# Kernel optimization log

Hardware: AMD Instinct MI355X
Metric: run time of the kernel (lower is better)

Reference implementation:

```python
import jax, jax.numpy as jnp
import numpy as np

DIM_V, DIM_T, DIM_OUT, NUM_HEADS = 1024, 1024, 1024, 16
HEAD_DIM = DIM_OUT // NUM_HEADS
BETA = 1.0  # module multiplies scores by self.beta (=1); self.scale is unused


def setup_inputs() -> dict:
    key = jax.random.key(0)
    ks = jax.random.split(key, 12)
    B, N1, N2 = 8, 256, 4096
    E = jax.random.normal(ks[0], (B, N1, DIM_T), dtype=jnp.float32)
    I = jax.random.normal(ks[1], (B, N2, DIM_V), dtype=jnp.float32)
    s = 0.02
    # Conv1d(kernel_size=1) == linear; weights stored [out, in], bias [out]
    q_w = jax.random.normal(ks[2], (DIM_OUT, DIM_T), dtype=jnp.float32) * s
    q_b = jnp.zeros((DIM_OUT,), dtype=jnp.float32)
    k_w = jax.random.normal(ks[3], (DIM_OUT, DIM_V), dtype=jnp.float32) * s
    k_b = jnp.zeros((DIM_OUT,), dtype=jnp.float32)
    v_w = jax.random.normal(ks[4], (DIM_OUT, DIM_V), dtype=jnp.float32) * s
    v_b = jnp.zeros((DIM_OUT,), dtype=jnp.float32)
    p_w = jax.random.normal(ks[5], (DIM_OUT, DIM_OUT), dtype=jnp.float32) * s
    p_b = jnp.zeros((DIM_OUT,), dtype=jnp.float32)
    return {"E": E, "I": I, "q_w": q_w, "q_b": q_b, "k_w": k_w, "k_b": k_b,
            "v_w": v_w, "v_b": v_b, "p_w": p_w, "p_b": p_b}


def reference(E, I, q_w, q_b, k_w, k_b, v_w, v_b, p_w, p_b):
    B, N1, _ = E.shape
    _, N2, _ = I.shape
    # 1x1 conv projections == dense layers over channel dim
    Q = (jnp.einsum('bnc,oc->bno', E, q_w) + q_b).reshape(B, N1, NUM_HEADS, HEAD_DIM)
    K = (jnp.einsum('bmc,oc->bmo', I, k_w) + k_b).reshape(B, N2, NUM_HEADS, HEAD_DIM)
    V = (jnp.einsum('bmc,oc->bmo', I, v_w) + v_b).reshape(B, N2, NUM_HEADS, HEAD_DIM)
    # cross-attention scores [B, H, N1, N2]
    attn = jnp.einsum('bnhd,bmhd->bhnm', Q, K) * BETA
    attn = jax.nn.softmax(attn, axis=-1)
    U = jnp.einsum('bhnm,bmhd->bnhd', attn, V).reshape(B, N1, DIM_OUT)
    U = jnp.einsum('bnc,oc->bno', U, p_w) + p_b
    U = U / jnp.linalg.norm(U, axis=-1, keepdims=True)
    return jnp.concatenate([E, U], axis=2)  # [B, N1, dim_t + dim_out]
```

## Files before the change

### kernel.cpp

```cpp
#include <hip/hip_runtime.h>
#include <hip/hip_bf16.h>
#include <stdint.h>


typedef __bf16 bf16_t;
typedef __attribute__((ext_vector_type(8))) __bf16 bf16x8;
typedef __attribute__((ext_vector_type(4))) __bf16 bf16x4;
typedef __attribute__((ext_vector_type(4))) float f32x4;

#define DEVINL __device__ __forceinline__

DEVINL f32x4 mfma16(bf16x8 a, bf16x8 b, f32x4 c) {
  return __builtin_amdgcn_mfma_f32_16x16x32_bf16(a, b, c, 0, 0, 0);
}

DEVINL float fexp2(float x) { return __builtin_exp2f(x); }

DEVINL bf16x8 load8(const bf16_t* p) { return *(const bf16x8*)p; }
DEVINL bf16x8 load8(const float* p) {
  const float4 u = *(const float4*)p;
  const float4 v = *(const float4*)(p + 4);
  bf16x8 r;
  r[0] = (bf16_t)u.x; r[1] = (bf16_t)u.y; r[2] = (bf16_t)u.z; r[3] = (bf16_t)u.w;
  r[4] = (bf16_t)v.x; r[5] = (bf16_t)v.y; r[6] = (bf16_t)v.z; r[7] = (bf16_t)v.w;
  return r;
}

DEVINL uint32_t pack_bf16(float a, float b) {
  union { bf16_t h[2]; uint32_t u; } x;
  x.h[0] = (bf16_t)a; x.h[1] = (bf16_t)b;
  return x.u;
}

DEVINL void async16(const void* g, void* l) {
  typedef const __attribute__((address_space(1))) unsigned int* gp1;
  typedef __attribute__((address_space(3))) unsigned int* lp3;
  __builtin_amdgcn_global_load_lds((gp1)(uintptr_t)g,
                                   (lp3)(uint32_t)(uintptr_t)l, 16, 0, 0);
}

__global__ __launch_bounds__(256) void cvt_f32_bf16(
    const float* __restrict__ src, bf16_t* __restrict__ dst, int n8) {
  const int i = blockIdx.x * 256 + threadIdx.x;
  if (i < n8) *(bf16x8*)(dst + (size_t)i * 8) = load8(src + (size_t)i * 8);
}

template <int MODE>
__global__ __launch_bounds__(256) void gemm_bt_async(
    const bf16_t* __restrict__ A, const bf16_t* __restrict__ B,
    const float* __restrict__ bias, bf16_t* __restrict__ C,
    int M, int N, int K) {
  __shared__ bf16_t As[2][128 * 32];
  __shared__ bf16_t Bs[2][128 * 32];
  const int tid = threadIdx.x;
  const int w = tid >> 6, lane = tid & 63, quad = lane >> 4, l16 = lane & 15;
  const int bid = blockIdx.x;
  const int swz = (bid & 7) * (int)(gridDim.x >> 3) + (bid >> 3);
  const int big = swz >> 3, small = swz & 7;
  const int bm = 128 * (MODE == 1 ? small : big);
  const int bn = 128 * (MODE == 1 ? big : small);
  const int wm = (w & 1) * 64, wn = (w >> 1) * 64;
  const int srow = tid >> 2;
  const int sw8 = ((tid & 3) ^ (srow & 3)) * 8;

  const bf16_t* Ag0 = A + (size_t)(bm + srow) * K + sw8;
  const bf16_t* Ag1 = Ag0 + (size_t)64 * K;
  const bf16_t* Bg0 = B + (size_t)(bn + srow) * K + sw8;
  const bf16_t* Bg1 = Bg0 + (size_t)64 * K;

  f32x4 acc[4][4] = {};

  for (int k0 = 0; k0 < K; k0 += 64) {
    async16(Ag0 + k0, As[0] + tid * 8);
    async16(Ag1 + k0, As[0] + 64 * 32 + tid * 8);
    async16(Bg0 + k0, Bs[0] + tid * 8);
    async16(Bg1 + k0, Bs[0] + 64 * 32 + tid * 8);
    async16(Ag0 + k0 + 32, As[1] + tid * 8);
    async16(Ag1 + k0 + 32, As[1] + 64 * 32 + tid * 8);
    async16(Bg0 + k0 + 32, Bs[1] + tid * 8);
    async16(Bg1 + k0 + 32, Bs[1] + 64 * 32 + tid * 8);
    __syncthreads();
#pragma unroll
    for (int h = 0; h < 2; h++) {
      bf16x8 af[4], bfr[4];
#pragma unroll
      for (int mt = 0; mt < 4; mt++) {
        const int r = wm + mt * 16 + l16;
        af[mt] = *(const bf16x8*)(As[h] + r * 32 + ((quad ^ (r & 3)) * 8));
      }
#pragma unroll
      for (int nt = 0; nt < 4; nt++) {
        const int r = wn + nt * 16 + l16;
        bfr[nt] = *(const bf16x8*)(Bs[h] + r * 32 + ((quad ^ (r & 3)) * 8));
      }
#pragma unroll
      for (int mt = 0; mt < 4; mt++)
#pragma unroll
        for (int nt = 0; nt < 4; nt++)
          acc[mt][nt] = mfma16(af[mt], bfr[nt], acc[mt][nt]);
    }
    __syncthreads();
  }

#pragma unroll
  for (int mt = 0; mt < 4; mt++) {
#pragma unroll
    for (int nt = 0; nt < 4; nt++) {
      const int gm0 = bm + wm + mt * 16 + quad * 4;
      const int gn = bn + wn + nt * 16 + l16;
#pragma unroll
      for (int r = 0; r < 4; r++) {
        const int gm = gm0 + r;
        C[(size_t)gm * N + gn] =
            (bf16_t)(acc[mt][nt][r] + bias[MODE == 1 ? gm : gn]);
      }
    }
  }
}

template <int MODE, typename TA, typename TB>
__global__ __launch_bounds__(256) void gemm_bt_reg(
    const TA* __restrict__ A, const TB* __restrict__ B,
    const float* __restrict__ bias, void* __restrict__ Cv,
    int M, int N, int K) {
  __shared__ bf16_t As[128 * 32];
  __shared__ bf16_t Bs[128 * 32];
  const int tid = threadIdx.x;
  const int w = tid >> 6, lane = tid & 63, quad = lane >> 4, l16 = lane & 15;
  const int bm = blockIdx.x * 128, bn = blockIdx.y * 128;
  const int wm = (w & 1) * 64, wn = (w >> 1) * 64;
  const int srow = tid >> 2;
  const int swz = ((tid & 3) ^ (srow & 3)) * 8;

  const TA* Ag0 = A + (size_t)(bm + srow) * K + swz;
  const TA* Ag1 = Ag0 + (size_t)64 * K;
  const TB* Bg0 = B + (size_t)(bn + srow) * K + swz;
  const TB* Bg1 = Bg0 + (size_t)64 * K;
  bf16_t* Al0 = As + tid * 8;
  bf16_t* Al1 = As + 64 * 32 + tid * 8;
  bf16_t* Bl0 = Bs + tid * 8;
  bf16_t* Bl1 = Bs + 64 * 32 + tid * 8;

  f32x4 acc[4][4] = {};

  for (int k0 = 0; k0 < K; k0 += 32) {
    const bf16x8 a0 = load8(Ag0 + k0);
    const bf16x8 a1 = load8(Ag1 + k0);
    const bf16x8 b0 = load8(Bg0 + k0);
    const bf16x8 b1 = load8(Bg1 + k0);
    *(bf16x8*)Al0 = a0;
    *(bf16x8*)Al1 = a1;
    *(bf16x8*)Bl0 = b0;
    *(bf16x8*)Bl1 = b1;
    __syncthreads();
    bf16x8 af[4], bfr[4];
#pragma unroll
    for (int mt = 0; mt < 4; mt++) {
      const int r = wm + mt * 16 + l16;
      af[mt] = *(const bf16x8*)(As + r * 32 + ((quad ^ (r & 3)) * 8));
    }
#pragma unroll
    for (int nt = 0; nt < 4; nt++) {
      const int r = wn + nt * 16 + l16;
      bfr[nt] = *(const bf16x8*)(Bs + r * 32 + ((quad ^ (r & 3)) * 8));
    }
#pragma unroll
    for (int mt = 0; mt < 4; mt++)
#pragma unroll
      for (int nt = 0; nt < 4; nt++)
        acc[mt][nt] = mfma16(af[mt], bfr[nt], acc[mt][nt]);
    __syncthreads();
  }

#pragma unroll
  for (int mt = 0; mt < 4; mt++) {
#pragma unroll
    for (int nt = 0; nt < 4; nt++) {
      const int gm0 = bm + wm + mt * 16 + quad * 4;
      const int gn = bn + wn + nt * 16 + l16;
#pragma unroll
      for (int r = 0; r < 4; r++) {
        const int gm = gm0 + r;
        float v = acc[mt][nt][r] + bias[MODE == 1 ? gm : gn];
        if (MODE == 3) v *= 1.4426950408889634f;
        if (MODE == 2)
          ((float*)Cv)[(size_t)gm * N + gn] = v;
        else
          ((bf16_t*)Cv)[(size_t)gm * N + gn] = (bf16_t)v;
      }
    }
  }
}

DEVINL void attn_step2(bf16x8 ke0, bf16x8 ke1, bf16x8 ko0, bf16x8 ko1,
                       const bf16x8 (&vf)[4],
                       const bf16x8 (&qf0)[2], const bf16x8 (&qf1)[2],
                       f32x4 (&o)[4][2], float (&lacc)[2]) {
  const f32x4 cm44 = {-44.f, -44.f, -44.f, -44.f};
#pragma unroll
  for (int qg = 0; qg < 2; qg++) {
    f32x4 z0 = cm44;
    z0 = mfma16(ke0, qf0[qg], z0);
    const f32x4 ste = mfma16(ke1, qf1[qg], z0);
    f32x4 z1 = cm44;
    z1 = mfma16(ko0, qf0[qg], z1);
    const f32x4 sto = mfma16(ko1, qf1[qg], z1);
    const float pe0 = fexp2(ste[0]), pe1 = fexp2(ste[1]);
    const float pe2 = fexp2(ste[2]), pe3 = fexp2(ste[3]);
    const float po0 = fexp2(sto[0]), po1 = fexp2(sto[1]);
    const float po2 = fexp2(sto[2]), po3 = fexp2(sto[3]);
    lacc[qg] += ((pe0 + pe1) + (pe2 + pe3)) + ((po0 + po1) + (po2 + po3));
    union { uint32_t u[4]; bf16x8 v; } pb;
    pb.u[0] = pack_bf16(pe0, pe1);
    pb.u[1] = pack_bf16(pe2, pe3);
    pb.u[2] = pack_bf16(po0, po1);
    pb.u[3] = pack_bf16(po2, po3);
    o[0][qg] = mfma16(vf[0], pb.v, o[0][qg]);
    o[1][qg] = mfma16(vf[1], pb.v, o[1][qg]);
    o[2][qg] = mfma16(vf[2], pb.v, o[2][qg]);
    o[3][qg] = mfma16(vf[3], pb.v, o[3][qg]);
  }
}

__global__ __launch_bounds__(512, 4) void attn_regs(
    const bf16_t* __restrict__ QU, const bf16_t* __restrict__ Kbuf,
    const bf16_t* __restrict__ Vtbuf, float* __restrict__ opart,
    float* __restrict__ mls) {
  __shared__ __attribute__((aligned(16))) char smem[35840];
  bf16_t* Ks = (bf16_t*)smem;
  bf16_t* Vs = (bf16_t*)(smem + 16384);
  float* lo = (float*)smem;
  float* ll = (float*)(smem + 34816);
  const int tid = threadIdx.x;
  const int w = tid >> 6, lane = tid & 63, quad = lane >> 4, l16 = lane & 15;
  const int wq = w >> 1, wk = w & 1, xr = l16 & 7;
  const int flat = blockIdx.x;
  const int qt = flat >> 9, s = (flat >> 7) & 3, h = (flat >> 3) & 15, b = flat & 7;

  bf16x8 qf0[2], qf1[2];
  const bf16_t* qb =
      QU + (size_t)(b * 256 + qt * 128 + wq * 32 + l16) * 1024 + h * 64 + quad * 8;
#pragma unroll
  for (int qg = 0; qg < 2; qg++) {
    qf0[qg] = *(const bf16x8*)(qb + (size_t)qg * 16 * 1024);
    qf1[qg] = *(const bf16x8*)(qb + (size_t)qg * 16 * 1024 + 32);
  }

  const int krow = tid >> 3;
  const int ksc = (tid & 7) ^ (krow & 7);
  const int vrow = tid >> 4;
  const int vsc = (tid & 15) ^ (vrow & 7);
  const bf16_t* ksrc0 =
      Kbuf + (size_t)(b * 4096 + s * 1024 + krow) * 1024 + h * 64 + ksc * 8;
  const bf16_t* ksrc1 = ksrc0 + (size_t)64 * 1024;
  const bf16_t* vsrc0 =
      Vtbuf + (size_t)(h * 64 + vrow) * 32768 + b * 4096 + s * 1024 + vsc * 8;
  const bf16_t* vsrc1 = vsrc0 + (size_t)32 * 32768;

  f32x4 o[4][2] = {};
  float lacc[2] = {};

  for (int it = 0; it < 8; it++) {
    async16(ksrc0, Ks + tid * 8);
    async16(ksrc1, Ks + 4096 + tid * 8);
    async16(vsrc0, Vs + tid * 8);
    async16(vsrc1, Vs + 4096 + tid * 8);
    ksrc0 += (size_t)128 * 1024;
    ksrc1 += (size_t)128 * 1024;
    vsrc0 += 128;
    vsrc1 += 128;
    __syncthreads();
#pragma unroll
    for (int sub = 0; sub < 2; sub++) {
      const int rowe = wk * 64 + sub * 32 + l16, rowo = rowe + 16;
      const bf16x8 ke0 = *(const bf16x8*)(Ks + rowe * 64 + ((quad ^ xr) * 8));
      const bf16x8 ke1 =
          *(const bf16x8*)(Ks + rowe * 64 + (((quad + 4) ^ xr) * 8));
      const bf16x8 ko0 = *(const bf16x8*)(Ks + rowo * 64 + ((quad ^ xr) * 8));
      const bf16x8 ko1 =
          *(const bf16x8*)(Ks + rowo * 64 + (((quad + 4) ^ xr) * 8));
      bf16x8 vf[4];
      const int c8 = wk * 8 + sub * 4 + (quad >> 1), in4 = (quad & 1) * 4;
#pragma unroll
      for (int dt = 0; dt < 4; dt++) {
        const int vr = dt * 16 + l16;
        union { bf16x4 h4[2]; bf16x8 v; } u;
        u.h4[0] = *(const bf16x4*)(Vs + vr * 128 + ((c8 ^ xr) * 8) + in4);
        u.h4[1] =
            *(const bf16x4*)(Vs + vr * 128 + (((c8 + 2) ^ xr) * 8) + in4);
        vf[dt] = u.v;
      }
      attn_step2(ke0, ke1, ko0, ko1, vf, qf0, qf1, o, lacc);
    }
    __syncthreads();
  }

#pragma unroll
  for (int qg = 0; qg < 2; qg++) {
    lacc[qg] += __shfl_xor(lacc[qg], 16);
    lacc[qg] += __shfl_xor(lacc[qg], 32);
  }
  if (quad == 0) {
#pragma unroll
    for (int qg = 0; qg < 2; qg++) ll[wk * 128 + wq * 32 + qg * 16 + l16] = lacc[qg];
  }
  if (wk == 0) {
#pragma unroll
    for (int qg = 0; qg < 2; qg++)
#pragma unroll
      for (int dt = 0; dt < 4; dt++)
        *(f32x4*)&lo[(wq * 32 + qg * 16 + l16) * 68 + dt * 16 + quad * 4] =
            o[dt][qg];
  }
  __syncthreads();
  if (wk == 1) {
    const int pr0 = ((b * 16 + h) << 8) | (qt * 128 + wq * 32);
#pragma unroll
    for (int qg = 0; qg < 2; qg++) {
      const int q = wq * 32 + qg * 16 + l16;
      const int pr = pr0 + qg * 16 + l16;
#pragma unroll
      for (int dt = 0; dt < 4; dt++) {
        f32x4 t = *(const f32x4*)&lo[q * 68 + dt * 16 + quad * 4];
        t = t + o[dt][qg];
        *(f32x4*)(opart + ((size_t)s * 32768 + pr) * 64 + dt * 16 + quad * 4) = t;
      }
      if (quad == 0) mls[(size_t)s * 32768 + pr] = ll[q] + ll[128 + q];
    }
  }
}

__global__ __launch_bounds__(256) void attn_combine(
    const float* __restrict__ opart, const float* __restrict__ mls,
    bf16_t* __restrict__ QU) {
  const int w = threadIdx.x >> 6, lane = threadIdx.x & 63;
  const int pr = blockIdx.x * 4 + w;
  float L = 0.f, acc = 0.f;
#pragma unroll
  for (int s = 0; s < 4; s++) {
    L += mls[(size_t)s * 32768 + pr];
    acc += opart[((size_t)s * 32768 + pr) * 64 + lane];
  }
  const int b = pr >> 12, h = (pr >> 8) & 15, q = pr & 255;
  QU[(size_t)(b * 256 + q) * 1024 + h * 64 + lane] =
      (bf16_t)(acc / fmaxf(L, 1e-37f));
}

__global__ __launch_bounds__(256) void attn_old(
    bf16_t* QU, const bf16_t* __restrict__ Kbuf,
    const bf16_t* __restrict__ Vtbuf, int hg, int G, int Kst) {
  __shared__ bf16_t Ks[64 * 64];
  __shared__ bf16_t Vs[64 * 64];
  __shared__ bf16_t Ps[4][16 * 64];
  const int tid = threadIdx.x;
  const int w = tid >> 6, lane = tid & 63, quad = lane >> 4, l16 = lane & 15;
  const int flat = blockIdx.x;
  const int qt = flat / (8 * G);
  const int rem = flat - qt * 8 * G;
  const int hh = rem % G, b = rem / G;
  const int h = hg + hh;

  const int qrow = b * 256 + qt * 64 + w * 16 + l16;
  const bf16_t* qbase = QU + (size_t)qrow * 1024 + h * 64 + quad * 8;
  const bf16x8 qf0 = *(const bf16x8*)(qbase);
  const bf16x8 qf1 = *(const bf16x8*)(qbase + 32);

  const int srow = tid >> 3;
  const int swz = ((tid & 7) ^ (srow & 7)) * 8;
  const bf16_t* Kg = Kbuf + (size_t)(b * 4096 + srow) * Kst + hh * 64 + swz;
  const bf16_t* Vg = Vtbuf + (size_t)(hh * 64 + srow) * 32768 + b * 4096 + swz;

  f32x4 o[4] = {};
  float mrow[4] = {-1e30f, -1e30f, -1e30f, -1e30f};
  float lrow[4] = {0.f, 0.f, 0.f, 0.f};
  const float L2E = 1.4426950408889634f;

  bf16x8 kv0 = *(const bf16x8*)(Kg);
  bf16x8 kv1 = *(const bf16x8*)(Kg + (size_t)32 * Kst);
  bf16x8 vv0 = *(const bf16x8*)(Vg);
  bf16x8 vv1 = *(const bf16x8*)(Vg + (size_t)32 * 32768);

  for (int kt = 0; kt < 64; kt++) {
    __syncthreads();
    *(bf16x8*)(Ks + tid * 8) = kv0;
    *(bf16x8*)(Ks + 32 * 64 + tid * 8) = kv1;
    *(bf16x8*)(Vs + tid * 8) = vv0;
    *(bf16x8*)(Vs + 32 * 64 + tid * 8) = vv1;
    __syncthreads();
    if (kt < 63) {
      const size_t ko = (size_t)(kt + 1) * 64;
      kv0 = *(const bf16x8*)(Kg + ko * Kst);
      kv1 = *(const bf16x8*)(Kg + (ko + 32) * Kst);
      vv0 = *(const bf16x8*)(Vg + ko);
      vv1 = *(const bf16x8*)(Vg + ko + (size_t)32 * 32768);
    }

    f32x4 s[4];
#pragma unroll
    for (int nt = 0; nt < 4; nt++) {
      const int key = nt * 16 + l16;
      const bf16x8 kf0 = *(const bf16x8*)(Ks + key * 64 + ((quad ^ (key & 7)) * 8));
      const bf16x8 kf1 = *(const bf16x8*)(Ks + key * 64 + (((quad + 4) ^ (key & 7)) * 8));
      f32x4 z = {0.f, 0.f, 0.f, 0.f};
      z = mfma16(qf0, kf0, z);
      s[nt] = mfma16(qf1, kf1, z);
    }

    float mnew[4], alpha[4], rsum[4];
#pragma unroll
    for (int r = 0; r < 4; r++) {
      float mx = fmaxf(fmaxf(s[0][r], s[1][r]), fmaxf(s[2][r], s[3][r]));
      mx = fmaxf(mx, __shfl_xor(mx, 1));
      mx = fmaxf(mx, __shfl_xor(mx, 2));
      mx = fmaxf(mx, __shfl_xor(mx, 4));
      mx = fmaxf(mx, __shfl_xor(mx, 8));
      mnew[r] = fmaxf(mrow[r], mx);
      alpha[r] = exp2f((mrow[r] - mnew[r]) * L2E);
      rsum[r] = 0.f;
    }
#pragma unroll
    for (int nt = 0; nt < 4; nt++) {
      const int key = nt * 16 + l16;
#pragma unroll
      for (int r = 0; r < 4; r++) {
        const float p = exp2f((s[nt][r] - mnew[r]) * L2E);
        rsum[r] += p;
        const int q = quad * 4 + r;
        Ps[w][q * 64 + (((key >> 3) ^ (q & 7)) * 8) + (key & 7)] = (bf16_t)p;
      }
    }
#pragma unroll
    for (int r = 0; r < 4; r++) {
      rsum[r] += __shfl_xor(rsum[r], 1);
      rsum[r] += __shfl_xor(rsum[r], 2);
      rsum[r] += __shfl_xor(rsum[r], 4);
      rsum[r] += __shfl_xor(rsum[r], 8);
      lrow[r] = lrow[r] * alpha[r] + rsum[r];
      mrow[r] = mnew[r];
    }
#pragma unroll
    for (int nt = 0; nt < 4; nt++) {
      o[nt][0] *= alpha[0]; o[nt][1] *= alpha[1];
      o[nt][2] *= alpha[2]; o[nt][3] *= alpha[3];
    }

    __syncthreads();

    const bf16x8 pf0 = *(const bf16x8*)(&Ps[w][l16 * 64 + ((quad ^ (l16 & 7)) * 8)]);
    const bf16x8 pf1 = *(const bf16x8*)(&Ps[w][l16 * 64 + (((quad + 4) ^ (l16 & 7)) * 8)]);
#pragma unroll
    for (int nt = 0; nt < 4; nt++) {
      const int d = nt * 16 + l16;
      const bf16x8 vf0 = *(const bf16x8*)(Vs + d * 64 + ((quad ^ (d & 7)) * 8));
      const bf16x8 vf1 = *(const bf16x8*)(Vs + d * 64 + (((quad + 4) ^ (d & 7)) * 8));
      o[nt] = mfma16(pf0, vf0, o[nt]);
      o[nt] = mfma16(pf1, vf1, o[nt]);
    }
  }

  float inv[4];
#pragma unroll
  for (int r = 0; r < 4; r++) inv[r] = 1.0f / fmaxf(lrow[r], 1e-30f);
#pragma unroll
  for (int nt = 0; nt < 4; nt++) {
#pragma unroll
    for (int r = 0; r < 4; r++) {
      const int row = b * 256 + qt * 64 + w * 16 + quad * 4 + r;
      QU[(size_t)row * 1024 + h * 64 + nt * 16 + l16] = (bf16_t)(o[nt][r] * inv[r]);
    }
  }
}

__global__ __launch_bounds__(256) void norm_concat(
    const float* __restrict__ E, const float* __restrict__ P,
    float* __restrict__ out) {
  const int row = blockIdx.x, tid = threadIdx.x;
  const int w = tid >> 6, lane = tid & 63;

  *(float4*)(out + (size_t)row * 2048 + tid * 4) =
      *(const float4*)(E + (size_t)row * 1024 + tid * 4);

  const float4 p = *(const float4*)(P + (size_t)row * 1024 + tid * 4);
  float ss = p.x * p.x + p.y * p.y + p.z * p.z + p.w * p.w;
#pragma unroll
  for (int m = 1; m <= 32; m <<= 1) ss += __shfl_xor(ss, m);
  __shared__ float red[4];
  if (lane == 0) red[w] = ss;
  __syncthreads();
  const float rn = rsqrtf(fmaxf(red[0] + red[1] + red[2] + red[3], 1e-30f));
  float4 q;
  q.x = p.x * rn; q.y = p.y * rn; q.z = p.z * rn; q.w = p.w * rn;
  *(float4*)(out + (size_t)row * 2048 + 1024 + tid * 4) = q;
}

extern "C" void kernel_launch(void* const* d_in, const int* in_sizes, int n_in,
                              void* d_out, int out_size, void* d_ws, size_t ws_size,
                              hipStream_t stream) {
  (void)in_sizes; (void)n_in; (void)out_size;
  const float* E   = (const float*)d_in[0];
  const float* I   = (const float*)d_in[1];
  const float* q_w = (const float*)d_in[2];
  const float* q_b = (const float*)d_in[3];
  const float* k_w = (const float*)d_in[4];
  const float* k_b = (const float*)d_in[5];
  const float* v_w = (const float*)d_in[6];
  const float* v_b = (const float*)d_in[7];
  const float* p_w = (const float*)d_in[8];
  const float* p_b = (const float*)d_in[9];
  float* out = (float*)d_out;
  char* ws = (char*)d_ws;

  if (ws_size >= (200ull << 20)) {
    bf16_t* QU    = (bf16_t*)(ws);
    bf16_t* k_wbf = (bf16_t*)(ws + (4u << 20));
    bf16_t* v_wbf = (bf16_t*)(ws + (6u << 20));
    bf16_t* Ibf   = (bf16_t*)(ws + (8u << 20));
    float*  Pf    = (float*)(ws + (8u << 20));
    float*  opart = (float*)(ws + (16u << 20));
    float*  mls   = (float*)(ws + (52u << 20));
    bf16_t* Kbuf  = (bf16_t*)(ws + (72u << 20));
    bf16_t* Vtbuf = (bf16_t*)(ws + (136u << 20));

    cvt_f32_bf16<<<16384, 256, 0, stream>>>(I, Ibf, 32768 * 1024 / 8);
    cvt_f32_bf16<<<512, 256, 0, stream>>>(k_w, k_wbf, 1024 * 1024 / 8);
    cvt_f32_bf16<<<512, 256, 0, stream>>>(v_w, v_wbf, 1024 * 1024 / 8);

    gemm_bt_reg<3, float, float><<<dim3(16, 8), 256, 0, stream>>>(
        E, q_w, q_b, QU, 2048, 1024, 1024);
    gemm_bt_async<0><<<2048, 256, 0, stream>>>(
        Ibf, k_wbf, k_b, Kbuf, 32768, 1024, 1024);
    gemm_bt_async<1><<<2048, 256, 0, stream>>>(
        v_wbf, Ibf, v_b, Vtbuf, 1024, 32768, 1024);
    attn_regs<<<1024, 512, 0, stream>>>(QU, Kbuf, Vtbuf, opart, mls);
    attn_combine<<<8192, 256, 0, stream>>>(opart, mls, QU);
    gemm_bt_reg<2, bf16_t, float><<<dim3(16, 8), 256, 0, stream>>>(
        QU, p_w, p_b, Pf, 2048, 1024, 1024);
    norm_concat<<<2048, 256, 0, stream>>>(E, Pf, out);
  } else {
    int G = 2;
    if (ws_size >= (133ull << 20)) G = 16;
    else if (ws_size >= (69ull << 20)) G = 8;
    else if (ws_size >= (37ull << 20)) G = 4;
    bf16_t* QU    = (bf16_t*)(ws);
    bf16_t* Kbuf  = (bf16_t*)(ws + (4u << 20));
    bf16_t* Vtbuf = (bf16_t*)(ws + (4u << 20) + ((size_t)G << 22));
    float*  Pf    = (float*)(ws + (4u << 20));

    gemm_bt_reg<0, float, float><<<dim3(16, 8), 256, 0, stream>>>(
        E, q_w, q_b, QU, 2048, 1024, 1024);
    for (int hg = 0; hg < 16; hg += G) {
      const int Nh = G * 64;
      gemm_bt_reg<0, float, float><<<dim3(256, Nh / 128), 256, 0, stream>>>(
          I, k_w + (size_t)hg * 64 * 1024, k_b + hg * 64, Kbuf, 32768, Nh, 1024);
      gemm_bt_reg<1, float, float><<<dim3(Nh / 128, 256), 256, 0, stream>>>(
          v_w + (size_t)hg * 64 * 1024, I, v_b + hg * 64, Vtbuf, Nh, 32768, 1024);
      attn_old<<<32 * G, 256, 0, stream>>>(QU, Kbuf, Vtbuf, hg, G, Nh);
    }
    gemm_bt_reg<2, bf16_t, float><<<dim3(16, 8), 256, 0, stream>>>(
        QU, p_w, p_b, Pf, 2048, 1024, 1024);
    norm_concat<<<2048, 256, 0, stream>>>(E, Pf, out);
  }
}
```

Measured before the change: 559.5 us.

## Double-buffer async GEMM LDS tiles and register-prefetch next K tile in sync GEMM

The async GEMM now keeps two 128x64 LDS buffers per operand. It issues the global_load_lds for the next K tile before computing on the current one and uses a wider 8-way XOR swizzle. The register-staged GEMM prefetches the next K slice into registers while the current one is being computed. Both changes aim to hide global-memory latency behind MFMA work, at the cost of doubled LDS use (64KB) and more registers, which may lower occupancy.

After: 548.7 us. No clear change (-1.9%).

```diff
diff --git a/kernel.cpp b/kernel.cpp
--- a/kernel.cpp
+++ b/kernel.cpp
@@ -50,8 +50,8 @@
     const bf16_t* __restrict__ A, const bf16_t* __restrict__ B,
     const float* __restrict__ bias, bf16_t* __restrict__ C,
     int M, int N, int K) {
-  __shared__ bf16_t As[2][128 * 32];
-  __shared__ bf16_t Bs[2][128 * 32];
+  __shared__ bf16_t As[2][128 * 64];
+  __shared__ bf16_t Bs[2][128 * 64];
   const int tid = threadIdx.x;
   const int w = tid >> 6, lane = tid & 63, quad = lane >> 4, l16 = lane & 15;
   const int bid = blockIdx.x;
@@ -60,47 +60,54 @@
   const int bm = 128 * (MODE == 1 ? small : big);
   const int bn = 128 * (MODE == 1 ? big : small);
   const int wm = (w & 1) * 64, wn = (w >> 1) * 64;
-  const int srow = tid >> 2;
-  const int sw8 = ((tid & 3) ^ (srow & 3)) * 8;
-
-  const bf16_t* Ag0 = A + (size_t)(bm + srow) * K + sw8;
-  const bf16_t* Ag1 = Ag0 + (size_t)64 * K;
-  const bf16_t* Bg0 = B + (size_t)(bn + srow) * K + sw8;
-  const bf16_t* Bg1 = Bg0 + (size_t)64 * K;
+  const int srow = tid >> 3;
+  const int sc8 = ((tid & 7) ^ (srow & 7)) * 8;
+
+  const bf16_t* Ag = A + (size_t)(bm + srow) * K + sc8;
+  const bf16_t* Bg = B + (size_t)(bn + srow) * K + sc8;
 
   f32x4 acc[4][4] = {};
 
+#define STAGE_TILE(buf, k0)                                              \
+  {                                                                      \
+    _Pragma("unroll") for (int c = 0; c < 4; c++) {                      \
+      async16(Ag + (size_t)(c * 32) * K + (k0), As[buf] + c * 2048 + tid * 8); \
+      async16(Bg + (size_t)(c * 32) * K + (k0), Bs[buf] + c * 2048 + tid * 8); \
+    }                                                                    \
+  }
+
+  STAGE_TILE(0, 0);
+  __syncthreads();
+  int cur = 0;
+
   for (int k0 = 0; k0 < K; k0 += 64) {
-    async16(Ag0 + k0, As[0] + tid * 8);
-    async16(Ag1 + k0, As[0] + 64 * 32 + tid * 8);
-    async16(Bg0 + k0, Bs[0] + tid * 8);
-    async16(Bg1 + k0, Bs[0] + 64 * 32 + tid * 8);
-    async16(Ag0 + k0 + 32, As[1] + tid * 8);
-    async16(Ag1 + k0 + 32, As[1] + 64 * 32 + tid * 8);
-    async16(Bg0 + k0 + 32, Bs[1] + tid * 8);
-    async16(Bg1 + k0 + 32, Bs[1] + 64 * 32 + tid * 8);
-    __syncthreads();
-#pragma unroll
-    for (int h = 0; h < 2; h++) {
-      bf16x8 af[4], bfr[4];
-#pragma unroll
-      for (int mt = 0; mt < 4; mt++) {
-        const int r = wm + mt * 16 + l16;
-        af[mt] = *(const bf16x8*)(As[h] + r * 32 + ((quad ^ (r & 3)) * 8));
+    if (k0 + 64 < K) STAGE_TILE(cur ^ 1, k0 + 64);
+    bf16x8 af0[4], af1[4], bf0[4], bf1[4];
+#pragma unroll
+    for (int mt = 0; mt < 4; mt++) {
+      const int r = wm + mt * 16 + l16;
+      af0[mt] = *(const bf16x8*)(As[cur] + r * 64 + ((quad ^ (r & 7)) * 8));
+      af1[mt] =
+          *(const bf16x8*)(As[cur] + r * 64 + (((quad + 4) ^ (r & 7)) * 8));
+    }
+#pragma unroll
+    for (int nt = 0; nt < 4; nt++) {
+      const int r = wn + nt * 16 + l16;
+      bf0[nt] = *(const bf16x8*)(Bs[cur] + r * 64 + ((quad ^ (r & 7)) * 8));
+      bf1[nt] =
+          *(const bf16x8*)(Bs[cur] + r * 64 + (((quad + 4) ^ (r & 7)) * 8));
+    }
+#pragma unroll
+    for (int mt = 0; mt < 4; mt++)
+#pragma unroll
+      for (int nt = 0; nt < 4; nt++) {
+        acc[mt][nt] = mfma16(af0[mt], bf0[nt], acc[mt][nt]);
+        acc[mt][nt] = mfma16(af1[mt], bf1[nt], acc[mt][nt]);
       }
-#pragma unroll
-      for (int nt = 0; nt < 4; nt++) {
-        const int r = wn + nt * 16 + l16;
-        bfr[nt] = *(const bf16x8*)(Bs[h] + r * 32 + ((quad ^ (r & 3)) * 8));
-      }
-#pragma unroll
-      for (int mt = 0; mt < 4; mt++)
-#pragma unroll
-        for (int nt = 0; nt < 4; nt++)
-          acc[mt][nt] = mfma16(af[mt], bfr[nt], acc[mt][nt]);
-    }
-    __syncthreads();
-  }
+    __syncthreads();
+    cur ^= 1;
+  }
+#undef STAGE_TILE
 
 #pragma unroll
   for (int mt = 0; mt < 4; mt++) {
@@ -143,16 +150,21 @@
 
   f32x4 acc[4][4] = {};
 
+  bf16x8 a0 = load8(Ag0), a1 = load8(Ag1);
+  bf16x8 b0 = load8(Bg0), b1 = load8(Bg1);
+
   for (int k0 = 0; k0 < K; k0 += 32) {
-    const bf16x8 a0 = load8(Ag0 + k0);
-    const bf16x8 a1 = load8(Ag1 + k0);
-    const bf16x8 b0 = load8(Bg0 + k0);
-    const bf16x8 b1 = load8(Bg1 + k0);
     *(bf16x8*)Al0 = a0;
     *(bf16x8*)Al1 = a1;
     *(bf16x8*)Bl0 = b0;
     *(bf16x8*)Bl1 = b1;
     __syncthreads();
+    if (k0 + 32 < K) {
+      a0 = load8(Ag0 + k0 + 32);
+      a1 = load8(Ag1 + k0 + 32);
+      b0 = load8(Bg0 + k0 + 32);
+      b1 = load8(Bg1 + k0 + 32);
+    }
     bf16x8 af[4], bfr[4];
 #pragma unroll
     for (int mt = 0; mt < 4; mt++) {
```
